# Kernel optimization log

Measured on AMD Instinct MI355X. Metric: run time of the kernel, lower is better.

## Reference

```python
import jax, jax.numpy as jnp
import numpy as np

N, S, V, DEG, K, HID = 4096, 128, 32, 32, 8, 64
E = N * DEG
LAMBDA_ATTN = 0.55


def setup_inputs():
    key = jax.random.key(0)
    ks = jax.random.split(key, 16)
    def w(k, shape, fan_in):
        return jax.random.normal(k, shape, jnp.float32) / np.float32(np.sqrt(fan_in))
    return {
        "h_s": jax.random.normal(ks[0], (N, S), jnp.float32),
        "h_v": jax.random.normal(ks[1], (N, V, 3), jnp.float32),
        "pos": jax.random.normal(ks[2], (N, 3), jnp.float32),
        "edge_index": jax.random.randint(ks[3], (2, E), 0, N),
        "batch": jnp.zeros((N,), jnp.int32),
        "W1": w(ks[4], (S, S), S),
        "Wg": w(ks[5], (S, 2 * V), S),
        "W2": w(ks[6], (S, S), S),
        "Wm1": w(ks[7], (S, HID), S), "bm1": jnp.zeros((HID,), jnp.float32),
        "Wm2": w(ks[8], (HID, 1), HID), "bm2": jnp.zeros((1,), jnp.float32),
        "Wq": w(ks[9], (S, S), S), "Wk": w(ks[10], (S, S), S),
        "Wa1": w(ks[11], (3 * S, S), 3 * S), "ba1": jnp.zeros((S,), jnp.float32),
        "Wa2": w(ks[12], (S, 1), S), "ba2": jnp.zeros((1,), jnp.float32),
    }


def _edge_feats(pos, src, dst):
    # vectors src - dst, length-expanded scalar attr [E,S], direction vector attr [E,V,3]
    vec = pos[src] - pos[dst]
    ln = jnp.linalg.norm(vec, axis=-1, keepdims=True)
    dirn = jnp.where(ln > 1e-12, vec / jnp.maximum(ln, 1e-12), 0.0)  # nan_to_num
    es = jnp.broadcast_to(ln, (src.shape[0], S))
    ev = jnp.broadcast_to(dirn[:, None, :], (src.shape[0], V, 3))
    return es, ev


def _scatter_softmax(scores, seg, n, validf):
    s = jnp.where(validf > 0, scores, -jnp.inf)
    mx = jax.ops.segment_max(s, seg, num_segments=n)
    mx = jnp.where(jnp.isfinite(mx), mx, 0.0)
    e = jnp.where(validf > 0, jnp.exp(s - mx[seg]), 0.0)
    den = jax.ops.segment_sum(e, seg, num_segments=n)
    return e / jnp.maximum(den[seg], 1e-9)


def _backbone(s, v, src, dst, es, ev, msg_mask, W1, Wg, W2):
    # gather-src gated messages, modulated by edge attrs, scatter-sum to dst
    m_s = jax.nn.relu(s[src] @ W1) * es                       # [E,S]
    g = s[src] @ Wg                                           # [E,2V]
    m_v = v[src] * g[:, :V, None] + ev * g[:, V:, None]       # [E,V,3]
    if msg_mask is not None:
        m_s = m_s * msg_mask[:, None]
        m_v = m_v * msg_mask[:, None, None]
    ds = jax.ops.segment_sum(m_s, dst, num_segments=N) @ W2
    dv = jax.ops.segment_sum(m_v, dst, num_segments=N)
    return ds, dv


def reference(h_s, h_v, pos, edge_index, batch, W1, Wg, W2, Wm1, bm1, Wm2, bm2, Wq, Wk, Wa1, ba1, Wa2, ba2):
    src, dst = edge_index[0], edge_index[1]
    # local message passing with residual
    es, ev = _edge_feats(pos, src, dst)
    ds, dv = _backbone(h_s, h_v, src, dst, es, ev, None, W1, Wg, W2)
    hl_s = h_s + ds
    hl_v = h_v + dv
    # master selection (soft score m, hard mask at 0.5)
    m = jax.nn.sigmoid((jax.nn.relu(hl_s @ Wm1 + bm1) @ Wm2 + bm2)[:, 0])
    mask = (m > 0.5).astype(hl_s.dtype)
    # virtual edge generation among master nodes (dense attention, thresholded)
    attn = jax.nn.sigmoid((hl_s @ Wq) @ (hl_s @ Wk).T / np.float32(np.sqrt(S)))  # [N,N]
    adj = jnp.zeros((N, N), hl_s.dtype).at[src, dst].add(1.0)
    mm = mask[:, None] * mask[None, :]
    allowed = (mm > 0) & (adj == 0) & (~jnp.eye(N, dtype=bool))
    vals, cols = jax.lax.top_k(jnp.where(allowed, attn, -jnp.inf), K)  # [N,K]
    vf = ((vals > LAMBDA_ATTN) & jnp.isfinite(vals)).astype(hl_s.dtype)
    rows = jnp.broadcast_to(jnp.arange(N)[:, None], (N, K))
    A_virtual = jnp.zeros((N, N), hl_s.dtype).at[rows, cols].add(vf)
    vsrc = rows.reshape(-1)
    vdst = cols.reshape(-1)
    vvf = vf.reshape(-1)
    # attention-based decay weights on virtual edges (scatter-softmax over dst)
    es_v, ev_v = _edge_feats(pos, vsrc, vdst)
    attn_in = jnp.concatenate([hl_s[vsrc], hl_s[vdst], es_v], axis=-1)  # [NK,3S]
    sc = (jax.nn.relu(attn_in @ Wa1 + ba1) @ Wa2 + ba2)[:, 0]
    decay = _scatter_softmax(sc, vdst, N, vvf)
    # hierarchical pass: induced master-master edges (w=1) + virtual edges (w=decay)
    asrc = jnp.concatenate([src, vsrc])
    adst = jnp.concatenate([dst, vdst])
    a_es = jnp.concatenate([es, es_v * decay[:, None]], axis=0)
    a_ev = jnp.concatenate([ev, ev_v * decay[:, None, None]], axis=0)
    amask = jnp.concatenate([mask[src] * mask[dst], vvf])
    dms, dmv = _backbone(hl_s, hl_v, asrc, adst, a_es, a_ev, amask, W1, Wg, W2)
    # expand hierarchical update to full node set (zero at non-masters), blend by m
    exp_s = mask[:, None] * (hl_s + dms)
    exp_v = mask[:, None, None] * (hl_v + dmv)
    hf_s = (1 - m[:, None]) * hl_s + m[:, None] * exp_s
    hf_v = (1 - m[:, None, None]) * hl_v + m[:, None, None] * exp_v
    return hf_s, hf_v, pos, A_virtual, m
```

## Files before the change

kernel.cpp:

```cpp
#include <hip/hip_runtime.h>
#include <math.h>

#define NN 4096
#define EE 131072
#define NKMAX 32768

#define SCALE_FX 8388608.0
#define INV_FX   (1.0/8388608.0)

__device__ __forceinline__ void atomAddFx(long long* p, float v) {
  atomicAdd((unsigned long long*)p, (unsigned long long)llrint((double)v * SCALE_FX));
}
__device__ __forceinline__ long long toFx(float v) {
  return llrint((double)v * SCALE_FX);
}
__device__ __forceinline__ float fxToF(long long v) {
  return (float)((double)v * INV_FX);
}

#define OFF_LN    ((size_t)0)
#define OFF_DIRN  (OFF_LN + EE)
#define OFF_R     (OFF_DIRN + (size_t)EE*3)
#define OFF_G     (OFF_R + (size_t)NN*128)
#define OFF_P1    (OFF_G + (size_t)NN*64)
#define OFF_HLS   (OFF_P1 + (size_t)NN*96)
#define OFF_HLV   (OFF_HLS + (size_t)NN*128)
#define OFF_MVAL  (OFF_HLV + (size_t)NN*96)
#define OFF_MASK  (OFF_MVAL + NN)
#define OFF_Q     (OFF_MASK + NN)
#define OFF_K     (OFF_Q + (size_t)NN*128)
#define OFF_A1    (OFF_K + (size_t)NN*128)
#define OFF_A2    (OFF_A1 + (size_t)NN*128)
#define OFF_R2    (OFF_A2 + (size_t)NN*128)
#define OFF_G2    (OFF_R2 + (size_t)NN*128)
#define OFF_P2    (OFF_G2 + (size_t)NN*64)
#define OFF_W3    (OFF_P2 + (size_t)NN*96)
#define OFF_LNV   (OFF_W3 + 128)
#define OFF_DIRV  (OFF_LNV + NKMAX)
#define OFF_SC    (OFF_DIRV + (size_t)NKMAX*3)
#define OFF_EEXP  (OFF_SC + NKMAX)
#define OFF_VEDGE (OFF_EEXP + NKMAX)
#define OFF_MIDX  (OFF_VEDGE + (size_t)NKMAX*2)
#define OFF_PT    (OFF_MIDX + NN)
#define OFF_CSR   (OFF_PT + (size_t)NN*32)
#define OFF_ROWPT (OFF_CSR + EE)
#define OFF_CURS  (OFF_ROWPT + NN + 64)
#define OFF_S1S   (OFF_CURS + NN)
#define OFF_S1V   (OFF_S1S + (size_t)NN*128)
#define OFF_S2S   OFF_R
#define OFF_S2V   OFF_P1
#define OFF_ZBEG  (OFF_S1V + (size_t)NN*96)
#define OFF_CNTH  (OFF_ZBEG)
#define OFF_ACCS  (OFF_CNTH + NN)
#define OFF_ACCV  (OFF_ACCS + (size_t)NN*256)
#define OFF_DEN64 (OFF_ACCV + (size_t)NN*192)
#define OFF_MX    (OFF_DEN64 + (size_t)NN*2)
#define OFF_ADJ   (OFF_MX + NN)
#define OFF_CNT   (OFF_ADJ + (size_t)NN*128)
#define OFF_END   (OFF_CNT + 64)

#define OUT_HFS 0
#define OUT_HFV 524288
#define OUT_POS 917504
#define OUT_AV  929792
#define OUT_M   17707008

#define INSERT8(TV, TC, VAL, IDX) do { \
  if ((VAL) > TV[7]) { \
    _Pragma("unroll") \
    for (int k_ = 7; k_ >= 1; --k_) { \
      bool gtk_ = (VAL) > TV[k_]; bool gtm_ = (VAL) > TV[k_-1]; \
      float nv_ = gtk_ ? (gtm_ ? TV[k_-1] : (VAL)) : TV[k_]; \
      int   ni_ = gtk_ ? (gtm_ ? TC[k_-1] : (IDX)) : TC[k_]; \
      TV[k_] = nv_; TC[k_] = ni_; } \
    bool gt0_ = (VAL) > TV[0]; \
    TV[0] = gt0_ ? (VAL) : TV[0]; TC[0] = gt0_ ? (IDX) : TC[0]; \
  } } while (0)

__device__ __forceinline__ void merge32(float (&tv)[8], int (&tc)[8]) {
  #pragma unroll
  for (int m = 1; m <= 16; m <<= 1) {
    float av[16]; int ac[16];
    #pragma unroll
    for (int k = 0; k < 8; ++k) { av[k] = tv[k]; ac[k] = tc[k]; }
    #pragma unroll
    for (int k = 0; k < 8; ++k) {
      av[8+k] = __shfl_xor(tv[7-k], m, 64);
      ac[8+k] = __shfl_xor(tc[7-k], m, 64);
    }
    #pragma unroll
    for (int d = 8; d >= 1; d >>= 1) {
      #pragma unroll
      for (int i = 0; i < 16; ++i) {
        if ((i & d) == 0) {
          const int jx = i + d;
          if (jx < 16) {
            bool sw = (av[i] < av[jx]) || (av[i] == av[jx] && ac[i] > ac[jx]);
            float t1 = sw ? av[jx] : av[i]; float t2 = sw ? av[i] : av[jx];
            int   u1 = sw ? ac[jx] : ac[i]; int   u2 = sw ? ac[i] : ac[jx];
            av[i] = t1; av[jx] = t2; ac[i] = u1; ac[jx] = u2;
          }
        }
      }
    }
    #pragma unroll
    for (int k = 0; k < 8; ++k) { tv[k] = av[k]; tc[k] = ac[k]; }
  }
}

__global__ void hmp_edge_prep(const int* __restrict__ ei, const float* __restrict__ pos,
                              float* __restrict__ ln, float* __restrict__ dirn,
                              unsigned long long* __restrict__ adj,
                              int* __restrict__ cnth) {
  int e = blockIdx.x * 256 + threadIdx.x;
  if (e >= EE) return;
  int s = ei[e], d = ei[EE + e];
  float vx = pos[s*3+0] - pos[d*3+0];
  float vy = pos[s*3+1] - pos[d*3+1];
  float vz = pos[s*3+2] - pos[d*3+2];
  float l = sqrtf(vx*vx + vy*vy + vz*vz);
  ln[e] = l;
  if (l > 1e-12f) {
    dirn[e*3+0] = vx / l; dirn[e*3+1] = vy / l; dirn[e*3+2] = vz / l;
  } else {
    dirn[e*3+0] = 0.f; dirn[e*3+1] = 0.f; dirn[e*3+2] = 0.f;
  }
  atomicOr(&adj[(size_t)s*64 + (d >> 6)], 1ULL << (d & 63));
  atomicAdd(&cnth[d], 1);
}

__global__ void hmp_csr_scan(const int* __restrict__ cnth, int* __restrict__ rowptr,
                             int* __restrict__ cursor) {
  __shared__ int ls[256];
  int tid = threadIdx.x;
  int base = tid * 16;
  int loc[16];
  int s = 0;
  #pragma unroll
  for (int i = 0; i < 16; ++i) { loc[i] = s; s += cnth[base + i]; }
  ls[tid] = s;
  __syncthreads();
  for (int off = 1; off < 256; off <<= 1) {
    int v = (tid >= off) ? ls[tid - off] : 0;
    __syncthreads();
    ls[tid] += v;
    __syncthreads();
  }
  int p = ls[tid] - s;
  #pragma unroll
  for (int i = 0; i < 16; ++i) {
    int rp = p + loc[i];
    rowptr[base + i] = rp;
    cursor[base + i] = rp;
  }
  if (tid == 255) rowptr[NN] = ls[255];
}

__global__ void hmp_csr_scatter(const int* __restrict__ ei, int* __restrict__ cursor,
                                int* __restrict__ csr) {
  int e = blockIdx.x * 256 + threadIdx.x;
  if (e >= EE) return;
  int d = ei[EE + e];
  int p = atomicAdd(&cursor[d], 1);
  csr[p] = e;
}

struct GemmJobs {
  const float* A;
  const float* W[6];
  float* C[6];
  int Nc[6];
  int act[6];
  const float* res;
  const float* mval;
  const float* maskf;
};

__global__ __launch_bounds__(256) void hmp_gemm_k128(GemmJobs P) {
  const int g = blockIdx.z;
  const int nc = P.Nc[g];
  if ((int)blockIdx.y * 64 >= nc) return;
  const float* __restrict__ W = P.W[g];
  float* __restrict__ C = P.C[g];
  const int act = P.act[g];
  __shared__ float As[32][68];
  __shared__ float Bs[32][64];
  const int tid = threadIdx.x;
  const int row0 = blockIdx.x * 64, col0 = blockIdx.y * 64;
  const int ty = tid >> 4, tx = tid & 15;
  float acc[4][4];
  #pragma unroll
  for (int i = 0; i < 4; ++i)
    #pragma unroll
    for (int j = 0; j < 4; ++j) acc[i][j] = 0.f;

  for (int kb = 0; kb < 4; ++kb) {
    #pragma unroll
    for (int q = 0; q < 2; ++q) {
      int f4 = tid + 256*q;
      int r = f4 >> 3, cg = f4 & 7;
      float4 av = *(const float4*)&P.A[(size_t)(row0+r)*128 + kb*32 + cg*4];
      As[cg*4+0][r] = av.x; As[cg*4+1][r] = av.y; As[cg*4+2][r] = av.z; As[cg*4+3][r] = av.w;
    }
    #pragma unroll
    for (int q = 0; q < 2; ++q) {
      int f4 = tid + 256*q;
      int kr = f4 >> 4, cg = f4 & 15;
      *(float4*)&Bs[kr][cg*4] = *(const float4*)&W[(size_t)(kb*32+kr)*nc + col0 + cg*4];
    }
    __syncthreads();
    #pragma unroll
    for (int kk = 0; kk < 32; ++kk) {
      float4 a = *(float4*)&As[kk][ty*4];
      float4 b = *(float4*)&Bs[kk][tx*4];
      acc[0][0] += a.x*b.x; acc[0][1] += a.x*b.y; acc[0][2] += a.x*b.z; acc[0][3] += a.x*b.w;
      acc[1][0] += a.y*b.x; acc[1][1] += a.y*b.y; acc[1][2] += a.y*b.z; acc[1][3] += a.y*b.w;
      acc[2][0] += a.z*b.x; acc[2][1] += a.z*b.y; acc[2][2] += a.z*b.z; acc[2][3] += a.z*b.w;
      acc[3][0] += a.w*b.x; acc[3][1] += a.w*b.y; acc[3][2] += a.w*b.z; acc[3][3] += a.w*b.w;
    }
    __syncthreads();
  }
  #pragma unroll
  for (int i = 0; i < 4; ++i) {
    int rr = row0 + ty*4 + i;
    float mv = 0.f, mk = 0.f;
    if (act == 3) { mv = P.mval[rr]; mk = P.maskf[rr]; }
    #pragma unroll
    for (int j = 0; j < 4; ++j) {
      int cc = col0 + tx*4 + j;
      float v = acc[i][j];
      if (act == 1) v = fmaxf(v, 0.f);
      else if (act == 2) v += P.res[(size_t)rr*128 + cc];
      else if (act == 3) {
        float hl = P.res[(size_t)rr*128 + cc];
        v = (1.f - mv)*hl + mv*mk*(hl + v);
      }
      C[(size_t)rr*nc + cc] = v;
    }
  }
}

__global__ void hmp_mul_p1(const float* __restrict__ hv, const float* __restrict__ G,
                           float* __restrict__ P1) {
  int i = blockIdx.x * 256 + threadIdx.x;
  if (i >= NN*96) return;
  int n = i / 96, q = i - n*96, v = q / 3;
  P1[i] = hv[i] * G[(size_t)n*64 + v];
}

__global__ void hmp_hlv_p2(const float* __restrict__ hv, const float* __restrict__ S1v,
                           const float* __restrict__ G2, float* __restrict__ hlv,
                           float* __restrict__ P2) {
  int i = blockIdx.x * 256 + threadIdx.x;
  if (i >= NN*96) return;
  int n = i / 96, q = i - n*96, v = q / 3;
  float x = hv[i] + S1v[i];
  hlv[i] = x;
  P2[i] = x * G2[(size_t)n*64 + v];
}

__global__ __launch_bounds__(256) void hmp_csr_msg_s(
    const int* __restrict__ csr, const int* __restrict__ rowptr,
    const int* __restrict__ ei, const float* __restrict__ ln,
    const float* __restrict__ R, const float* __restrict__ maskf,
    float* __restrict__ S) {
  int d = blockIdx.x * 4 + (threadIdx.x >> 6);
  int l = threadIdx.x & 63;
  if (d >= NN) return;
  long long a0 = 0, a1 = 0;
  if (!maskf || maskf[d] > 0.f) {
    int k1 = rowptr[d + 1];
    for (int k = rowptr[d]; k < k1; ++k) {
      int e = csr[k];
      int s = ei[e];
      if (maskf && maskf[s] == 0.f) continue;
      float w = ln[e];
      a0 += toFx(w * R[(size_t)s*128 + l]);
      a1 += toFx(w * R[(size_t)s*128 + 64 + l]);
    }
  }
  S[(size_t)d*128 + l]      = fxToF(a0);
  S[(size_t)d*128 + 64 + l] = fxToF(a1);
}

__global__ __launch_bounds__(256) void hmp_csr_msg_v(
    const int* __restrict__ csr, const int* __restrict__ rowptr,
    const int* __restrict__ ei, const float* __restrict__ dirn,
    const float* __restrict__ P, const float* __restrict__ G,
    const float* __restrict__ maskf, float* __restrict__ Sv) {
  int d = blockIdx.x * 4 + (threadIdx.x >> 6);
  int l = threadIdx.x & 63;
  if (d >= NN) return;
  const int v0 = l / 3, c0 = l - v0*3;
  const int q1 = 64 + l, v1 = q1 / 3, c1 = q1 - v1*3;
  long long a0 = 0, a1 = 0;
  if (!maskf || maskf[d] > 0.f) {
    int k1 = rowptr[d + 1];
    for (int k = rowptr[d]; k < k1; ++k) {
      int e = csr[k];
      int s = ei[e];
      if (maskf && maskf[s] == 0.f) continue;
      float m0 = P[(size_t)s*96 + l] + dirn[(size_t)e*3 + c0] * G[(size_t)s*64 + 32 + v0];
      a0 += toFx(m0);
      if (l < 32) {
        float m1 = P[(size_t)s*96 + q1] + dirn[(size_t)e*3 + c1] * G[(size_t)s*64 + 32 + v1];
        a1 += toFx(m1);
      }
    }
  }
  Sv[(size_t)d*96 + l] = fxToF(a0);
  if (l < 32) Sv[(size_t)d*96 + q1] = fxToF(a1);
}

__global__ __launch_bounds__(256) void hmp_master(const float* __restrict__ hls,
                                                  const float* __restrict__ Wm1,
                                                  const float* __restrict__ bm1,
                                                  const float* __restrict__ Wm2,
                                                  const float* __restrict__ bm2,
                                                  float* __restrict__ mval,
                                                  float* __restrict__ maskf,
                                                  float* __restrict__ out_m) {
  __shared__ float sW[128*64];
  __shared__ float sx[4][128];
  int tid = threadIdx.x;
  for (int i = tid; i < 8192; i += 256) sW[i] = Wm1[i];
  for (int i = tid; i < 512; i += 256) {
    int nn = i >> 7;
    sx[nn][i & 127] = hls[(size_t)(blockIdx.x*4 + nn)*128 + (i & 127)];
  }
  __syncthreads();
  int nl = tid >> 6, lane = tid & 63;
  int n = blockIdx.x * 4 + nl;
  float h = bm1[lane];
  for (int k = 0; k < 128; ++k) h += sx[nl][k] * sW[k*64 + lane];
  h = fmaxf(h, 0.f) * Wm2[lane];
  for (int off = 32; off; off >>= 1) h += __shfl_down(h, off, 64);
  if (lane == 0) {
    float logit = h + bm2[0];
    float mv = 1.f / (1.f + expf(-logit));
    mval[n] = mv;
    maskf[n] = (mv > 0.5f) ? 1.f : 0.f;
    out_m[n] = mv;
  }
}

__global__ void hmp_compact(const float* __restrict__ maskf, int* __restrict__ midx,
                            int* __restrict__ nmp) {
  __shared__ int ls[256];
  int tid = threadIdx.x;
  int base = tid * 16;
  int cnt = 0;
  #pragma unroll
  for (int i = 0; i < 16; ++i) cnt += (maskf[base + i] > 0.f) ? 1 : 0;
  ls[tid] = cnt;
  __syncthreads();
  for (int off = 1; off < 256; off <<= 1) {
    int v = (tid >= off) ? ls[tid - off] : 0;
    __syncthreads();
    ls[tid] += v;
    __syncthreads();
  }
  int p = ls[tid] - cnt;
  for (int i = 0; i < 16; ++i)
    if (maskf[base + i] > 0.f) midx[p++] = base + i;
  if (tid == 255) *nmp = ls[255];
}

__global__ void hmp_colsum_w3(const float* __restrict__ Wa1, float* __restrict__ w3) {
  int s = threadIdx.x;
  float acc = 0.f;
  for (int k = 0; k < 128; ++k) acc += Wa1[(size_t)(256 + k)*128 + s];
  w3[s] = acc;
}

__global__ __launch_bounds__(256) void hmp_attn3(const float* __restrict__ Q,
                                                 const float* __restrict__ Kk,
                                                 const unsigned long long* __restrict__ adj,
                                                 const int* __restrict__ midx,
                                                 const int* __restrict__ nmp,
                                                 int2* __restrict__ pt) {
  const int nm = *nmp;
  const int rowblk = blockIdx.x >> 1;
  const int split  = blockIdx.x & 1;
  const int row0 = rowblk * 8;
  if (row0 >= nm) return;

  __shared__ float sQ[8][132];
  __shared__ float sK[64][132];
  __shared__ int   sCI[64];
  __shared__ int   sRI[8];
  __shared__ unsigned long long sAdj[8][64];

  const int tid = threadIdx.x;
  {
    int rr = tid >> 5, c = tid & 31;
    int gr = row0 + rr;
    int ri = (gr < nm) ? midx[gr] : -1;
    float4 v; v.x = v.y = v.z = v.w = 0.f;
    if (ri >= 0) v = *(const float4*)&Q[(size_t)ri*128 + c*4];
    *(float4*)&sQ[rr][c*4] = v;
  }
  if (tid < 8) sRI[tid] = (row0 + tid < nm) ? midx[row0 + tid] : -1;
  #pragma unroll
  for (int q = 0; q < 2; ++q) {
    int i = tid + 256*q;
    int rr = i >> 6, w = i & 63;
    int gr = row0 + rr;
    int ri = (gr < nm) ? midx[gr] : -1;
    sAdj[rr][w] = (ri >= 0) ? adj[(size_t)ri*64 + w] : 0ULL;
  }

  const int ntiles = (nm + 63) >> 6;
  const int l = tid & 63, wv = tid >> 6;
  const int r = wv*2 + (l >> 5);
  const int c0 = l & 31, c1 = c0 + 32;

  float tv[8]; int tc[8];
  #pragma unroll
  for (int k = 0; k < 8; ++k) { tv[k] = -1.f; tc[k] = 0x7fffffff; }

  for (int t = split; t < ntiles; t += 2) {
    #pragma unroll
    for (int q = 0; q < 8; ++q) {
      int f4 = tid + 256*q;
      int rr = f4 >> 5, c = f4 & 31;
      int gc = t*64 + rr;
      int ci = (gc < nm) ? midx[gc] : -1;
      float4 v; v.x = v.y = v.z = v.w = 0.f;
      if (ci >= 0) v = *(const float4*)&Kk[(size_t)ci*128 + c*4];
      *(float4*)&sK[rr][c*4] = v;
    }
    if (tid < 64) sCI[tid] = (t*64 + tid < nm) ? midx[t*64 + tid] : -1;
    __syncthreads();

    float a0x=0,a0y=0,a0z=0,a0w=0, a1x=0,a1y=0,a1z=0,a1w=0;
    #pragma unroll
    for (int kk = 0; kk < 32; ++kk) {
      float4 qv = *(float4*)&sQ[r][kk*4];
      float4 k0 = *(float4*)&sK[c0][kk*4];
      float4 k1 = *(float4*)&sK[c1][kk*4];
      a0x += qv.x*k0.x; a0y += qv.y*k0.y; a0z += qv.z*k0.z; a0w += qv.w*k0.w;
      a1x += qv.x*k1.x; a1y += qv.y*k1.y; a1z += qv.z*k1.z; a1w += qv.w*k1.w;
    }
    float d0 = (a0x+a0y)+(a0z+a0w);
    float d1 = (a1x+a1y)+(a1z+a1w);

    const int ro = sRI[r];
    const int jo0 = sCI[c0], jo1 = sCI[c1];
    {
      bool ok = (jo0 >= 0) && (ro >= 0) && (jo0 != ro) &&
                !((sAdj[r][jo0 >> 6] >> (jo0 & 63)) & 1ULL);
      if (ok) {
        float z = d0 / 11.3137085f;
        float attn = 1.f / (1.f + expf(-z));
        INSERT8(tv, tc, attn, jo0);
      }
    }
    {
      bool ok = (jo1 >= 0) && (ro >= 0) && (jo1 != ro) &&
                !((sAdj[r][jo1 >> 6] >> (jo1 & 63)) & 1ULL);
      if (ok) {
        float z = d1 / 11.3137085f;
        float attn = 1.f / (1.f + expf(-z));
        INSERT8(tv, tc, attn, jo1);
      }
    }
    __syncthreads();
  }

  merge32(tv, tc);

  if ((l & 31) == 0) {
    int gr = row0 + r;
    #pragma unroll
    for (int k = 0; k < 8; ++k)
      pt[((size_t)gr*2 + split)*8 + k] = make_int2(__float_as_int(tv[k]), tc[k]);
  }
}

__global__ void hmp_topk_emit(const int2* __restrict__ pt, const int* __restrict__ midx,
                              const int* __restrict__ nmp, float* __restrict__ Avirt,
                              int2* __restrict__ vedges, int* __restrict__ vcnt) {
  int i = blockIdx.x * 256 + threadIdx.x;
  if (i >= *nmp) return;
  const int2* LA = pt + (size_t)i*16;
  const int2* LB = LA + 8;
  int a = 0, b = 0;
  int grow = midx[i];
  #pragma unroll
  for (int k = 0; k < 8; ++k) {
    int2 ca = LA[a];
    int2 cb = LB[b];
    float va = __int_as_float(ca.x), vb = __int_as_float(cb.x);
    bool pickA = (va > vb) || (va == vb && ca.y < cb.y);
    int2 sel = pickA ? ca : cb;
    if (pickA) ++a; else ++b;
    float v = __int_as_float(sel.x);
    if (v > 0.55f) {
      Avirt[(size_t)grow*NN + sel.y] = 1.f;
      int slot = atomicAdd(vcnt, 1);
      vedges[slot] = make_int2(grow, sel.y);
    }
  }
}

__global__ __launch_bounds__(256) void hmp_vedge_sc(const int2* __restrict__ ve,
                                                    const int* __restrict__ vcnt,
                                                    const float* __restrict__ pos,
                                                    const float* __restrict__ A1,
                                                    const float* __restrict__ A2,
                                                    const float* __restrict__ w3,
                                                    const float* __restrict__ ba1,
                                                    const float* __restrict__ Wa2,
                                                    const float* __restrict__ ba2,
                                                    float* __restrict__ lnv,
                                                    float* __restrict__ dirv,
                                                    float* __restrict__ sc,
                                                    unsigned int* __restrict__ mxenc) {
  int cnt = *vcnt;
  int lane = threadIdx.x & 63;
  for (int e = blockIdx.x * 4 + (threadIdx.x >> 6); e < cnt; e += gridDim.x * 4) {
    int2 ed = ve[e];
    int i = ed.x, j = ed.y;
    float vx = pos[i*3+0] - pos[j*3+0];
    float vy = pos[i*3+1] - pos[j*3+1];
    float vz = pos[i*3+2] - pos[j*3+2];
    float lval = sqrtf(vx*vx + vy*vy + vz*vz);
    float acc = 0.f;
    #pragma unroll
    for (int half = 0; half < 2; ++half) {
      int c = lane + half*64;
      float tq = A1[(size_t)i*128 + c] + A2[(size_t)j*128 + c] + lval*w3[c] + ba1[c];
      acc += fmaxf(tq, 0.f) * Wa2[c];
    }
    for (int off = 32; off; off >>= 1) acc += __shfl_down(acc, off, 64);
    if (lane == 0) {
      lnv[e] = lval;
      if (lval > 1e-12f) {
        dirv[e*3+0] = vx / lval; dirv[e*3+1] = vy / lval; dirv[e*3+2] = vz / lval;
      } else {
        dirv[e*3+0] = 0.f; dirv[e*3+1] = 0.f; dirv[e*3+2] = 0.f;
      }
      float s = acc + ba2[0];
      sc[e] = s;
      unsigned int bits = __float_as_uint(s);
      unsigned int enc = (bits & 0x80000000u) ? ~bits : (bits | 0x80000000u);
      atomicMax(&mxenc[j], enc);
    }
  }
}

__global__ void hmp_vexp(const int2* __restrict__ ve, const int* __restrict__ vcnt,
                         const float* __restrict__ sc, const unsigned int* __restrict__ mxenc,
                         float* __restrict__ eexp, long long* __restrict__ den64) {
  int cnt = *vcnt;
  for (int e = blockIdx.x * 256 + threadIdx.x; e < cnt; e += gridDim.x * 256) {
    int j = ve[e].y;
    unsigned int enc = mxenc[j];
    unsigned int bits = (enc & 0x80000000u) ? (enc & 0x7fffffffu) : ~enc;
    float mx = __uint_as_float(bits);
    float ex = expf(sc[e] - mx);
    eexp[e] = ex;
    atomAddFx(&den64[j], ex);
  }
}

__global__ void hmp_msgv_s(const int2* __restrict__ ve, const int* __restrict__ vcnt,
                           const float* __restrict__ eexp, const long long* __restrict__ den64,
                           const float* __restrict__ lnv, const float* __restrict__ R2,
                           long long* __restrict__ acc) {
  int total = (*vcnt) << 7;
  for (int idx = blockIdx.x * 256 + threadIdx.x; idx < total; idx += gridDim.x * 256) {
    int e = idx >> 7, c = idx & 127;
    int2 ed = ve[e];
    float denf = fxToF(den64[ed.y]);
    float decay = eexp[e] / fmaxf(denf, 1e-9f);
    atomAddFx(&acc[(size_t)ed.y*128 + c], lnv[e] * decay * R2[(size_t)ed.x*128 + c]);
  }
}

__global__ void hmp_msgv_v(const int2* __restrict__ ve, const int* __restrict__ vcnt,
                           const float* __restrict__ eexp, const long long* __restrict__ den64,
                           const float* __restrict__ dirv, const float* __restrict__ P2,
                           const float* __restrict__ G2, long long* __restrict__ acc) {
  int total = (*vcnt) * 96;
  for (int idx = blockIdx.x * 256 + threadIdx.x; idx < total; idx += gridDim.x * 256) {
    int e = idx / 96, q = idx - e*96;
    int v = q / 3, c = q - v*3;
    int2 ed = ve[e];
    float denf = fxToF(den64[ed.y]);
    float decay = eexp[e] / fmaxf(denf, 1e-9f);
    float msg = P2[(size_t)ed.x*96 + q] + dirv[(size_t)e*3 + c] * decay * G2[(size_t)ed.x*64 + 32 + v];
    atomAddFx(&acc[(size_t)ed.y*96 + q], msg);
  }
}

__global__ void hmp_comb(float* __restrict__ S, const long long* __restrict__ acc, int n) {
  int i = blockIdx.x * 256 + threadIdx.x;
  if (i < n) S[i] += fxToF(acc[i]);
}

__global__ void hmp_final_v(const float* __restrict__ hlv, const float* __restrict__ S2v,
                            const long long* __restrict__ accv,
                            const float* __restrict__ mval, const float* __restrict__ maskf,
                            float* __restrict__ out) {
  int idx = blockIdx.x * 256 + threadIdx.x;
  if (idx >= NN*96) return;
  int n = idx / 96;
  float mv = mval[n], mk = maskf[n];
  float x = hlv[idx];
  out[idx] = (1.f - mv)*x + mv*mk*(x + S2v[idx] + fxToF(accv[idx]));
}

extern "C" void kernel_launch(void* const* d_in, const int* in_sizes, int n_in,
                              void* d_out, int out_size, void* d_ws, size_t ws_size,
                              hipStream_t stream) {
  const float* h_s = (const float*)d_in[0];
  const float* h_v = (const float*)d_in[1];
  const float* pos = (const float*)d_in[2];
  const int*   ei  = (const int*)d_in[3];
  const float* W1  = (const float*)d_in[5];
  const float* Wg  = (const float*)d_in[6];
  const float* W2  = (const float*)d_in[7];
  const float* Wm1 = (const float*)d_in[8];
  const float* bm1 = (const float*)d_in[9];
  const float* Wm2 = (const float*)d_in[10];
  const float* bm2 = (const float*)d_in[11];
  const float* Wq  = (const float*)d_in[12];
  const float* Wk  = (const float*)d_in[13];
  const float* Wa1 = (const float*)d_in[14];
  const float* ba1 = (const float*)d_in[15];
  const float* Wa2 = (const float*)d_in[16];
  const float* ba2 = (const float*)d_in[17];

  if (ws_size < OFF_END * sizeof(float)) return;

  float* ws  = (float*)d_ws;
  float* out = (float*)d_out;

  float* ln   = ws + OFF_LN;
  float* dirn = ws + OFF_DIRN;
  float* R    = ws + OFF_R;
  float* G    = ws + OFF_G;
  float* P1   = ws + OFF_P1;
  float* hls  = ws + OFF_HLS;
  float* hlv  = ws + OFF_HLV;
  float* mval = ws + OFF_MVAL;
  float* mskf = ws + OFF_MASK;
  float* Qb   = ws + OFF_Q;
  float* Kb   = ws + OFF_K;
  float* A1   = ws + OFF_A1;
  float* A2   = ws + OFF_A2;
  float* R2   = ws + OFF_R2;
  float* G2   = ws + OFF_G2;
  float* P2   = ws + OFF_P2;
  float* w3   = ws + OFF_W3;
  float* lnv  = ws + OFF_LNV;
  float* dirv = ws + OFF_DIRV;
  float* sc   = ws + OFF_SC;
  float* eexp = ws + OFF_EEXP;
  int2*  vedg = (int2*)(ws + OFF_VEDGE);
  int*   midx = (int*)(ws + OFF_MIDX);
  int2*  pt   = (int2*)(ws + OFF_PT);
  int*   csr  = (int*)(ws + OFF_CSR);
  int*   rowp = (int*)(ws + OFF_ROWPT);
  int*   curs = (int*)(ws + OFF_CURS);
  float* S1s  = ws + OFF_S1S;
  float* S1v  = ws + OFF_S1V;
  float* S2s  = ws + OFF_S2S;
  float* S2v  = ws + OFF_S2V;
  int*   cnth = (int*)(ws + OFF_CNTH);
  long long* accs  = (long long*)(ws + OFF_ACCS);
  long long* accv  = (long long*)(ws + OFF_ACCV);
  long long* den64 = (long long*)(ws + OFF_DEN64);
  unsigned int* mxenc = (unsigned int*)(ws + OFF_MX);
  unsigned long long* adj = (unsigned long long*)(ws + OFF_ADJ);
  int*   cnts = (int*)(ws + OFF_CNT);
  int*   vcnt = cnts + 0;
  int*   nmp  = cnts + 2;

  hipMemsetAsync(ws + OFF_ZBEG, 0, (OFF_END - OFF_ZBEG) * sizeof(float), stream);
  hipMemsetAsync(out + OUT_AV, 0, (size_t)NN * NN * sizeof(float), stream);
  hipMemcpyAsync(out + OUT_POS, pos, (size_t)NN * 3 * sizeof(float),
                 hipMemcpyDeviceToDevice, stream);

  hmp_edge_prep<<<EE/256, 256, 0, stream>>>(ei, pos, ln, dirn, adj, cnth);
  hmp_csr_scan<<<1, 256, 0, stream>>>(cnth, rowp, curs);
  hmp_csr_scatter<<<EE/256, 256, 0, stream>>>(ei, curs, csr);

  {
    GemmJobs J = {};
    J.A = h_s;
    J.W[0] = W1; J.C[0] = R; J.Nc[0] = 128; J.act[0] = 1;
    J.W[1] = Wg; J.C[1] = G; J.Nc[1] = 64;  J.act[1] = 0;
    hmp_gemm_k128<<<dim3(64,2,2), 256, 0, stream>>>(J);
  }
  hmp_mul_p1<<<NN*96/256, 256, 0, stream>>>(h_v, G, P1);
  hmp_csr_msg_s<<<NN/4, 256, 0, stream>>>(csr, rowp, ei, ln, R, nullptr, S1s);
  hmp_csr_msg_v<<<NN/4, 256, 0, stream>>>(csr, rowp, ei, dirn, P1, G, nullptr, S1v);

  {
    GemmJobs J = {};
    J.A = S1s; J.res = h_s;
    J.W[0] = W2; J.C[0] = hls; J.Nc[0] = 128; J.act[0] = 2;
    hmp_gemm_k128<<<dim3(64,2,1), 256, 0, stream>>>(J);
  }

  hmp_master<<<NN/4, 256, 0, stream>>>(hls, Wm1, bm1, Wm2, bm2, mval, mskf, out + OUT_M);
  hmp_compact<<<1, 256, 0, stream>>>(mskf, midx, nmp);

  {
    GemmJobs J = {};
    J.A = hls;
    J.W[0] = Wq;          J.C[0] = Qb; J.Nc[0] = 128; J.act[0] = 0;
    J.W[1] = Wk;          J.C[1] = Kb; J.Nc[1] = 128; J.act[1] = 0;
    J.W[2] = Wa1;         J.C[2] = A1; J.Nc[2] = 128; J.act[2] = 0;
    J.W[3] = Wa1 + 16384; J.C[3] = A2; J.Nc[3] = 128; J.act[3] = 0;
    J.W[4] = W1;          J.C[4] = R2; J.Nc[4] = 128; J.act[4] = 1;
    J.W[5] = Wg;          J.C[5] = G2; J.Nc[5] = 64;  J.act[5] = 0;
    hmp_gemm_k128<<<dim3(64,2,6), 256, 0, stream>>>(J);
  }
  hmp_colsum_w3<<<1, 128, 0, stream>>>(Wa1, w3);
  hmp_hlv_p2<<<NN*96/256, 256, 0, stream>>>(h_v, S1v, G2, hlv, P2);

  hmp_attn3<<<(NN/8)*2, 256, 0, stream>>>(Qb, Kb, adj, midx, nmp, pt);
  hmp_topk_emit<<<NN/256, 256, 0, stream>>>(pt, midx, nmp, out + OUT_AV, vedg, vcnt);

  hmp_vedge_sc<<<512, 256, 0, stream>>>(vedg, vcnt, pos, A1, A2, w3, ba1, Wa2, ba2,
                                        lnv, dirv, sc, mxenc);
  hmp_vexp<<<128, 256, 0, stream>>>(vedg, vcnt, sc, mxenc, eexp, den64);

  hmp_csr_msg_s<<<NN/4, 256, 0, stream>>>(csr, rowp, ei, ln, R2, mskf, S2s);
  hmp_csr_msg_v<<<NN/4, 256, 0, stream>>>(csr, rowp, ei, dirn, P2, G2, mskf, S2v);
  hmp_msgv_s<<<1024, 256, 0, stream>>>(vedg, vcnt, eexp, den64, lnv, R2, accs);
  hmp_msgv_v<<<1024, 256, 0, stream>>>(vedg, vcnt, eexp, den64, dirv, P2, G2, accv);
  hmp_comb<<<NN*128/256, 256, 0, stream>>>(S2s, accs, NN*128);

  {
    GemmJobs J = {};
    J.A = S2s; J.res = hls; J.mval = mval; J.maskf = mskf;
    J.W[0] = W2; J.C[0] = out + OUT_HFS; J.Nc[0] = 128; J.act[0] = 3;
    hmp_gemm_k128<<<dim3(64,2,1), 256, 0, stream>>>(J);
  }
  hmp_final_v<<<NN*96/256, 256, 0, stream>>>(hlv, S2v, accv, mval, mskf, out + OUT_HFV);
}
```

Measured before the change: 475.4 us.

## Split attention top-k into tiled score GEMM and per-row top-k pass

```diff
diff --git a/kernel.cpp b/kernel.cpp
--- a/kernel.cpp
+++ b/kernel.cpp
@@ -42,7 +42,7 @@
 #define OFF_VEDGE (OFF_EEXP + NKMAX)
 #define OFF_MIDX  (OFF_VEDGE + (size_t)NKMAX*2)
 #define OFF_PT    (OFF_MIDX + NN)
-#define OFF_CSR   (OFF_PT + (size_t)NN*32)
+#define OFF_CSR   (OFF_PT + (size_t)NN*64)
 #define OFF_ROWPT (OFF_CSR + EE)
 #define OFF_CURS  (OFF_ROWPT + NN + 64)
 #define OFF_S1S   (OFF_CURS + NN)
@@ -77,9 +77,9 @@
     TV[0] = gt0_ ? (VAL) : TV[0]; TC[0] = gt0_ ? (IDX) : TC[0]; \
   } } while (0)
 
-__device__ __forceinline__ void merge32(float (&tv)[8], int (&tc)[8]) {
-  #pragma unroll
-  for (int m = 1; m <= 16; m <<= 1) {
+__device__ __forceinline__ void merge64(float (&tv)[8], int (&tc)[8]) {
+  #pragma unroll
+  for (int m = 1; m <= 32; m <<= 1) {
     float av[16]; int ac[16];
     #pragma unroll
     for (int k = 0; k < 8; ++k) { av[k] = tv[k]; ac[k] = tc[k]; }
@@ -373,133 +373,120 @@
   w3[s] = acc;
 }
 
-__global__ __launch_bounds__(256) void hmp_attn3(const float* __restrict__ Q,
+__global__ __launch_bounds__(256) void hmp_score(const float* __restrict__ Q,
                                                  const float* __restrict__ Kk,
                                                  const unsigned long long* __restrict__ adj,
                                                  const int* __restrict__ midx,
                                                  const int* __restrict__ nmp,
-                                                 int2* __restrict__ pt) {
+                                                 float* __restrict__ scores) {
   const int nm = *nmp;
-  const int rowblk = blockIdx.x >> 1;
-  const int split  = blockIdx.x & 1;
-  const int row0 = rowblk * 8;
-  if (row0 >= nm) return;
-
-  __shared__ float sQ[8][132];
-  __shared__ float sK[64][132];
-  __shared__ int   sCI[64];
-  __shared__ int   sRI[8];
-  __shared__ unsigned long long sAdj[8][64];
-
+  const int row0 = blockIdx.x * 64, col0 = blockIdx.y * 64;
+  if (row0 >= nm || col0 >= nm) return;
+
+  __shared__ float As[32][68];
+  __shared__ float Bs[32][68];
   const int tid = threadIdx.x;
-  {
-    int rr = tid >> 5, c = tid & 31;
-    int gr = row0 + rr;
-    int ri = (gr < nm) ? midx[gr] : -1;
-    float4 v; v.x = v.y = v.z = v.w = 0.f;
-    if (ri >= 0) v = *(const float4*)&Q[(size_t)ri*128 + c*4];
-    *(float4*)&sQ[rr][c*4] = v;
-  }
-  if (tid < 8) sRI[tid] = (row0 + tid < nm) ? midx[row0 + tid] : -1;
-  #pragma unroll
-  for (int q = 0; q < 2; ++q) {
-    int i = tid + 256*q;
-    int rr = i >> 6, w = i & 63;
-    int gr = row0 + rr;
-    int ri = (gr < nm) ? midx[gr] : -1;
-    sAdj[rr][w] = (ri >= 0) ? adj[(size_t)ri*64 + w] : 0ULL;
-  }
+  const int ty = tid >> 4, tx = tid & 15;
+  float acc[4][4];
+  #pragma unroll
+  for (int i = 0; i < 4; ++i)
+    #pragma unroll
+    for (int j = 0; j < 4; ++j) acc[i][j] = 0.f;
+
+  for (int kb = 0; kb < 4; ++kb) {
+    #pragma unroll
+    for (int q = 0; q < 2; ++q) {
+      int f4 = tid + 256*q;
+      int r = f4 >> 3, cg = f4 & 7;
+      int gr = row0 + r;
+      float4 av; av.x = av.y = av.z = av.w = 0.f;
+      if (gr < nm) {
+        int ri = midx[gr];
+        av = *(const float4*)&Q[(size_t)ri*128 + kb*32 + cg*4];
+      }
+      As[cg*4+0][r] = av.x; As[cg*4+1][r] = av.y; As[cg*4+2][r] = av.z; As[cg*4+3][r] = av.w;
+    }
+    #pragma unroll
+    for (int q = 0; q < 2; ++q) {
+      int f4 = tid + 256*q;
+      int r = f4 >> 3, cg = f4 & 7;
+      int gc = col0 + r;
+      float4 bv; bv.x = bv.y = bv.z = bv.w = 0.f;
+      if (gc < nm) {
+        int ci = midx[gc];
+        bv = *(const float4*)&Kk[(size_t)ci*128 + kb*32 + cg*4];
+      }
+      Bs[cg*4+0][r] = bv.x; Bs[cg*4+1][r] = bv.y; Bs[cg*4+2][r] = bv.z; Bs[cg*4+3][r] = bv.w;
+    }
+    __syncthreads();
+    #pragma unroll
+    for (int kk = 0; kk < 32; ++kk) {
+      float4 a = *(float4*)&As[kk][ty*4];
+      float4 b = *(float4*)&Bs[kk][tx*4];
+      acc[0][0] += a.x*b.x; acc[0][1] += a.x*b.y; acc[0][2] += a.x*b.z; acc[0][3] += a.x*b.w;
+      acc[1][0] += a.y*b.x; acc[1][1] += a.y*b.y; acc[1][2] += a.y*b.z; acc[1][3] += a.y*b.w;
+      acc[2][0] += a.z*b.x; acc[2][1] += a.z*b.y; acc[2][2] += a.z*b.z; acc[2][3] += a.z*b.w;
+      acc[3][0] += a.w*b.x; acc[3][1] += a.w*b.y; acc[3][2] += a.w*b.z; acc[3][3] += a.w*b.w;
+    }
+    __syncthreads();
+  }
+
+  #pragma unroll
+  for (int i = 0; i < 4; ++i) {
+    int gi = row0 + ty*4 + i;
+    if (gi >= nm) continue;
+    int ri = midx[gi];
+    #pragma unroll
+    for (int j = 0; j < 4; ++j) {
+      int gj = col0 + tx*4 + j;
+      if (gj >= nm || gj == gi) continue;
+      int rj = midx[gj];
+      bool conn = (adj[(size_t)ri*64 + (rj >> 6)] >> (rj & 63)) & 1ULL;
+      if (!conn) {
+        float z = acc[i][j] / 11.3137085f;
+        float s = 1.f / (1.f + expf(-z));
+        scores[(size_t)ri*NN + gj] = s;
+      }
+    }
+  }
+}
+
+__global__ __launch_bounds__(256) void hmp_topk2(float* __restrict__ scores,
+                                                 const int* __restrict__ midx,
+                                                 const int* __restrict__ nmp,
+                                                 int2* __restrict__ vedges,
+                                                 int* __restrict__ vcnt) {
+  const int nm = *nmp;
+  int i = blockIdx.x * 4 + (threadIdx.x >> 6);
+  int l = threadIdx.x & 63;
+  if (i >= nm) return;
+  int mi = midx[i];
+
+  float tv[8]; int tc[8];
+  #pragma unroll
+  for (int k = 0; k < 8; ++k) { tv[k] = -1.f; tc[k] = 0x7fffffff; }
 
   const int ntiles = (nm + 63) >> 6;
-  const int l = tid & 63, wv = tid >> 6;
-  const int r = wv*2 + (l >> 5);
-  const int c0 = l & 31, c1 = c0 + 32;
-
-  float tv[8]; int tc[8];
-  #pragma unroll
-  for (int k = 0; k < 8; ++k) { tv[k] = -1.f; tc[k] = 0x7fffffff; }
-
-  for (int t = split; t < ntiles; t += 2) {
-    #pragma unroll
-    for (int q = 0; q < 8; ++q) {
-      int f4 = tid + 256*q;
-      int rr = f4 >> 5, c = f4 & 31;
-      int gc = t*64 + rr;
-      int ci = (gc < nm) ? midx[gc] : -1;
-      float4 v; v.x = v.y = v.z = v.w = 0.f;
-      if (ci >= 0) v = *(const float4*)&Kk[(size_t)ci*128 + c*4];
-      *(float4*)&sK[rr][c*4] = v;
-    }
-    if (tid < 64) sCI[tid] = (t*64 + tid < nm) ? midx[t*64 + tid] : -1;
-    __syncthreads();
-
-    float a0x=0,a0y=0,a0z=0,a0w=0, a1x=0,a1y=0,a1z=0,a1w=0;
-    #pragma unroll
-    for (int kk = 0; kk < 32; ++kk) {
-      float4 qv = *(float4*)&sQ[r][kk*4];
-      float4 k0 = *(float4*)&sK[c0][kk*4];
-      float4 k1 = *(float4*)&sK[c1][kk*4];
-      a0x += qv.x*k0.x; a0y += qv.y*k0.y; a0z += qv.z*k0.z; a0w += qv.w*k0.w;
-      a1x += qv.x*k1.x; a1y += qv.y*k1.y; a1z += qv.z*k1.z; a1w += qv.w*k1.w;
-    }
-    float d0 = (a0x+a0y)+(a0z+a0w);
-    float d1 = (a1x+a1y)+(a1z+a1w);
-
-    const int ro = sRI[r];
-    const int jo0 = sCI[c0], jo1 = sCI[c1];
-    {
-      bool ok = (jo0 >= 0) && (ro >= 0) && (jo0 != ro) &&
-                !((sAdj[r][jo0 >> 6] >> (jo0 & 63)) & 1ULL);
-      if (ok) {
-        float z = d0 / 11.3137085f;
-        float attn = 1.f / (1.f + expf(-z));
-        INSERT8(tv, tc, attn, jo0);
+  for (int t = 0; t < ntiles; ++t) {
+    int j = t*64 + l;
+    if (j < nm) {
+      float s = scores[(size_t)mi*NN + j];
+      if (s > 0.f) INSERT8(tv, tc, s, j);
+    }
+  }
+  merge64(tv, tc);
+
+  for (int j = l; j < nm; j += 64) scores[(size_t)mi*NN + j] = 0.f;
+
+  if (l == 0) {
+    #pragma unroll
+    for (int k = 0; k < 8; ++k) {
+      if (tv[k] > 0.55f) {
+        int col = midx[tc[k]];
+        scores[(size_t)mi*NN + col] = 1.f;
+        int slot = atomicAdd(vcnt, 1);
+        vedges[slot] = make_int2(mi, col);
       }
-    }
-    {
-      bool ok = (jo1 >= 0) && (ro >= 0) && (jo1 != ro) &&
-                !((sAdj[r][jo1 >> 6] >> (jo1 & 63)) & 1ULL);
-      if (ok) {
-        float z = d1 / 11.3137085f;
-        float attn = 1.f / (1.f + expf(-z));
-        INSERT8(tv, tc, attn, jo1);
-      }
-    }
-    __syncthreads();
-  }
-
-  merge32(tv, tc);
-
-  if ((l & 31) == 0) {
-    int gr = row0 + r;
-    #pragma unroll
-    for (int k = 0; k < 8; ++k)
-      pt[((size_t)gr*2 + split)*8 + k] = make_int2(__float_as_int(tv[k]), tc[k]);
-  }
-}
-
-__global__ void hmp_topk_emit(const int2* __restrict__ pt, const int* __restrict__ midx,
-                              const int* __restrict__ nmp, float* __restrict__ Avirt,
-                              int2* __restrict__ vedges, int* __restrict__ vcnt) {
-  int i = blockIdx.x * 256 + threadIdx.x;
-  if (i >= *nmp) return;
-  const int2* LA = pt + (size_t)i*16;
-  const int2* LB = LA + 8;
-  int a = 0, b = 0;
-  int grow = midx[i];
-  #pragma unroll
-  for (int k = 0; k < 8; ++k) {
-    int2 ca = LA[a];
-    int2 cb = LB[b];
-    float va = __int_as_float(ca.x), vb = __int_as_float(cb.x);
-    bool pickA = (va > vb) || (va == vb && ca.y < cb.y);
-    int2 sel = pickA ? ca : cb;
-    if (pickA) ++a; else ++b;
-    float v = __int_as_float(sel.x);
-    if (v > 0.55f) {
-      Avirt[(size_t)grow*NN + sel.y] = 1.f;
-      int slot = atomicAdd(vcnt, 1);
-      vedges[slot] = make_int2(grow, sel.y);
     }
   }
 }
@@ -661,7 +648,6 @@
   float* eexp = ws + OFF_EEXP;
   int2*  vedg = (int2*)(ws + OFF_VEDGE);
   int*   midx = (int*)(ws + OFF_MIDX);
-  int2*  pt   = (int2*)(ws + OFF_PT);
   int*   csr  = (int*)(ws + OFF_CSR);
   int*   rowp = (int*)(ws + OFF_ROWPT);
   int*   curs = (int*)(ws + OFF_CURS);
@@ -723,8 +709,8 @@
   hmp_colsum_w3<<<1, 128, 0, stream>>>(Wa1, w3);
   hmp_hlv_p2<<<NN*96/256, 256, 0, stream>>>(h_v, S1v, G2, hlv, P2);
 
-  hmp_attn3<<<(NN/8)*2, 256, 0, stream>>>(Qb, Kb, adj, midx, nmp, pt);
-  hmp_topk_emit<<<NN/256, 256, 0, stream>>>(pt, midx, nmp, out + OUT_AV, vedg, vcnt);
+  hmp_score<<<dim3(NN/64, NN/64), 256, 0, stream>>>(Qb, Kb, adj, midx, nmp, out + OUT_AV);
+  hmp_topk2<<<NN/4, 256, 0, stream>>>(out + OUT_AV, midx, nmp, vedg, vcnt);
 
   hmp_vedge_sc<<<512, 256, 0, stream>>>(vedg, vcnt, pos, A1, A2, w3, ba1, Wa2, ba2,
                                         lnv, dirv, sc, mxenc);
```

New measurement: 691.9 us. 45.5% more time.
